# Optimization experiments

Measured on AMD Instinct MI355X. Metric: run time of the kernel, lower is better.

Reference implementation:

```python
import jax, jax.numpy as jnp
import numpy as np

U = 3      # kronecker_partitions
DP = 128   # kronecker_subdim
K = 32     # top_k_slots
B = 64


def setup_inputs() -> dict:
    key = jax.random.key(0)
    z = jax.random.normal(key, (B, U * DP), dtype=jnp.float32)
    log_tau = jnp.zeros((1,), dtype=jnp.float32)  # learned temperature param
    return {"z": z, "log_tau": log_tau}


def reference(z, log_tau):
    b = z.shape[0]
    parts = z.reshape(b, U, DP)                      # [B, U, d_p]
    tau = jnp.exp(log_tau)
    probs = jax.nn.softmax(parts / tau, axis=-1)     # per-partition softmax
    # Kronecker (outer) product across partitions -> [B, d_p^U]
    addr = probs[:, 0]
    for u in range(1, U):  # static loop over U=3 partitions
        addr = (addr[:, :, None] * probs[:, u][:, None, :]).reshape(b, -1)
    weights, indices = jax.lax.top_k(addr, K)        # [B, K] each
    return indices, weights
```

## Files before the change

### kernel.cpp

```cpp
#include <hip/hip_runtime.h>
#include <math.h>

namespace {

constexpr int NU    = 3;
constexpr int DPN   = 128;
constexpr int TOPK  = 32;
constexpr int NB    = 64;
constexpr int NCAND = 119;

__global__ __launch_bounds__(DPN) void kron_topk_kernel(
    const float* __restrict__ z, const float* __restrict__ log_tau,
    float* __restrict__ out) {
  const int row = blockIdx.x;
  const int tid = threadIdx.x;

  __shared__ __align__(16) float p[NU][DPN];
  __shared__ __align__(16) float red[NU][DPN];
  __shared__ float sval[NU][TOPK];
  __shared__ int   sidx[NU][TOPK];
  __shared__ __align__(16) float cval[DPN];
  __shared__ __align__(16) int   cidx[DPN];
  __shared__ float aval[TOPK];
  __shared__ int   aidx[TOPK];

  const float* zr = z + row * (NU * DPN);
  float x[NU];
#pragma unroll
  for (int u = 0; u < NU; ++u) x[u] = zr[u * DPN + tid];
  const float tau = expf(log_tau[0]);

  int rmap = 0, smap = 0;
  const bool cact = tid < NCAND;
  if (cact) {
    int t = tid, r = 0;
    while (true) {
      int cnt = TOPK / (r + 1);
      if (t < cnt) break;
      t -= cnt;
      ++r;
    }
    rmap = r;
    smap = t;
  }

  if (tau != 1.0f) {
#pragma unroll
    for (int u = 0; u < NU; ++u) x[u] /= tau;
  }
#pragma unroll
  for (int u = 0; u < NU; ++u) red[u][tid] = x[u];
  __syncthreads();
  for (int s = DPN / 2; s > 0; s >>= 1) {
    if (tid < s) {
#pragma unroll
      for (int u = 0; u < NU; ++u)
        red[u][tid] = fmaxf(red[u][tid], red[u][tid + s]);
    }
    __syncthreads();
  }
  float e[NU];
#pragma unroll
  for (int u = 0; u < NU; ++u) e[u] = expf(x[u] - red[u][0]);
  __syncthreads();
#pragma unroll
  for (int u = 0; u < NU; ++u) red[u][tid] = e[u];
  __syncthreads();
  for (int s = DPN / 2; s > 0; s >>= 1) {
    if (tid < s) {
#pragma unroll
      for (int u = 0; u < NU; ++u) red[u][tid] += red[u][tid + s];
    }
    __syncthreads();
  }
  float pv[NU];
#pragma unroll
  for (int u = 0; u < NU; ++u) {
    pv[u] = e[u] / red[u][0];
    p[u][tid] = pv[u];
  }
  __syncthreads();

  {
    int rk[NU] = {0, 0, 0};
    const float4* p4_0 = reinterpret_cast<const float4*>(&p[0][0]);
    const float4* p4_1 = reinterpret_cast<const float4*>(&p[1][0]);
    const float4* p4_2 = reinterpret_cast<const float4*>(&p[2][0]);
#pragma unroll 8
    for (int jj = 0; jj < DPN / 4; ++jj) {
      float4 w0 = p4_0[jj];
      float4 w1 = p4_1[jj];
      float4 w2 = p4_2[jj];
      const float* w0e = &w0.x;
      const float* w1e = &w1.x;
      const float* w2e = &w2.x;
#pragma unroll
      for (int ee = 0; ee < 4; ++ee) {
        int j = 4 * jj + ee;
        rk[0] += (w0e[ee] > pv[0]) || (w0e[ee] == pv[0] && j < tid);
        rk[1] += (w1e[ee] > pv[1]) || (w1e[ee] == pv[1] && j < tid);
        rk[2] += (w2e[ee] > pv[2]) || (w2e[ee] == pv[2] && j < tid);
      }
    }
#pragma unroll
    for (int u = 0; u < NU; ++u)
      if (rk[u] < TOPK) { sval[u][rk[u]] = pv[u]; sidx[u][rk[u]] = tid; }
  }
  __syncthreads();

  if (tid < TOPK) { aval[tid] = sval[0][tid]; aidx[tid] = sidx[0][tid]; }
  __syncthreads();

  for (int u = 1; u < NU; ++u) {
    float v = -1.0f;
    int idx = 0x7fffffff;
    if (cact) {
      v   = aval[rmap] * sval[u][smap];
      idx = aidx[rmap] * DPN + sidx[u][smap];
    }
    cval[tid] = v;
    cidx[tid] = idx;
    __syncthreads();

    int rank = 0;
    const float4* cv4 = reinterpret_cast<const float4*>(cval);
    const int4*   ci4 = reinterpret_cast<const int4*>(cidx);
#pragma unroll 8
    for (int jj = 0; jj < DPN / 4; ++jj) {
      float4 w4 = cv4[jj];
      int4   i4 = ci4[jj];
      const float* we = &w4.x;
      const int*   ie = &i4.x;
#pragma unroll
      for (int ee = 0; ee < 4; ++ee)
        rank += (we[ee] > v) || (we[ee] == v && ie[ee] < idx);
    }
    __syncthreads();
    if (rank < TOPK) { aval[rank] = v; aidx[rank] = idx; }
    __syncthreads();
  }

  if (tid < TOPK) {
    out[row * TOPK + tid]              = (float)aidx[tid];
    out[NB * TOPK + row * TOPK + tid]  = aval[tid];
  }
}

}

extern "C" void kernel_launch(void* const* d_in, const int* in_sizes, int n_in,
                              void* d_out, int out_size, void* d_ws, size_t ws_size,
                              hipStream_t stream) {
  const float* z       = (const float*)d_in[0];
  const float* log_tau = (const float*)d_in[1];
  float* out           = (float*)d_out;
  hipLaunchKernelGGL(kron_topk_kernel, dim3(NB), dim3(DPN), 0, stream,
                     z, log_tau, out);
}
```

Baseline: 75.29 us.

## Use wave shuffles for softmax reductions and single-wave candidate merge

Replaces the shared-memory tree reductions for per-partition max and sum with wavefront shuffle reductions, which removes many block barriers. After the per-partition top-k, the second wave exits and the first wave handles all 119 candidates alone, two per lane. Block-wide syncs are replaced with LDS waitcnt fences. This cuts barrier and latency overhead in a tiny latency-bound kernel, at the cost of doubling the per-lane rank work in the merge phase and relying on wave-synchronous LDS semantics.

```diff
diff --git a/kernel.cpp b/kernel.cpp
--- a/kernel.cpp
+++ b/kernel.cpp
@@ -9,14 +9,34 @@
 constexpr int NB    = 64;
 constexpr int NCAND = 119;
 
+__device__ __forceinline__ void lds_fence() {
+  asm volatile("s_waitcnt lgkmcnt(0)" ::: "memory");
+  __builtin_amdgcn_sched_barrier(0);
+}
+
+__device__ __forceinline__ void decode_rs(int c, int& r, int& s) {
+  int t = c, rr = 0;
+  while (true) {
+    int cnt = TOPK / (rr + 1);
+    if (t < cnt) break;
+    t -= cnt;
+    ++rr;
+  }
+  r = rr;
+  s = t;
+}
+
 __global__ __launch_bounds__(DPN) void kron_topk_kernel(
     const float* __restrict__ z, const float* __restrict__ log_tau,
     float* __restrict__ out) {
-  const int row = blockIdx.x;
-  const int tid = threadIdx.x;
+  const int row  = blockIdx.x;
+  const int tid  = threadIdx.x;
+  const int lane = tid & 63;
+  const int wid  = tid >> 6;
 
+  __shared__ __align__(16) float es[NU][DPN];
   __shared__ __align__(16) float p[NU][DPN];
-  __shared__ __align__(16) float red[NU][DPN];
+  __shared__ float mxs[NU][2];
   __shared__ float sval[NU][TOPK];
   __shared__ int   sidx[NU][TOPK];
   __shared__ __align__(16) float cval[DPN];
@@ -29,54 +49,40 @@
 #pragma unroll
   for (int u = 0; u < NU; ++u) x[u] = zr[u * DPN + tid];
   const float tau = expf(log_tau[0]);
-
-  int rmap = 0, smap = 0;
-  const bool cact = tid < NCAND;
-  if (cact) {
-    int t = tid, r = 0;
-    while (true) {
-      int cnt = TOPK / (r + 1);
-      if (t < cnt) break;
-      t -= cnt;
-      ++r;
-    }
-    rmap = r;
-    smap = t;
-  }
-
   if (tau != 1.0f) {
 #pragma unroll
     for (int u = 0; u < NU; ++u) x[u] /= tau;
   }
+
+  float mm[NU] = {x[0], x[1], x[2]};
 #pragma unroll
-  for (int u = 0; u < NU; ++u) red[u][tid] = x[u];
+  for (int d = 32; d > 0; d >>= 1) {
+#pragma unroll
+    for (int u = 0; u < NU; ++u) mm[u] = fmaxf(mm[u], __shfl_xor(mm[u], d));
+  }
+  if (lane == 0) {
+#pragma unroll
+    for (int u = 0; u < NU; ++u) mxs[u][wid] = mm[u];
+  }
   __syncthreads();
-  for (int s = DPN / 2; s > 0; s >>= 1) {
-    if (tid < s) {
-#pragma unroll
-      for (int u = 0; u < NU; ++u)
-        red[u][tid] = fmaxf(red[u][tid], red[u][tid + s]);
-    }
-    __syncthreads();
-  }
+
   float e[NU];
 #pragma unroll
-  for (int u = 0; u < NU; ++u) e[u] = expf(x[u] - red[u][0]);
+  for (int u = 0; u < NU; ++u) {
+    float m = fmaxf(mxs[u][0], mxs[u][1]);
+    e[u] = expf(x[u] - m);
+    es[u][tid] = e[u];
+  }
   __syncthreads();
-#pragma unroll
-  for (int u = 0; u < NU; ++u) red[u][tid] = e[u];
-  __syncthreads();
-  for (int s = DPN / 2; s > 0; s >>= 1) {
-    if (tid < s) {
-#pragma unroll
-      for (int u = 0; u < NU; ++u) red[u][tid] += red[u][tid + s];
-    }
-    __syncthreads();
-  }
+
   float pv[NU];
 #pragma unroll
   for (int u = 0; u < NU; ++u) {
-    pv[u] = e[u] / red[u][0];
+    float v = es[u][lane] + es[u][lane + 64];
+#pragma unroll
+    for (int d = 32; d > 0; d >>= 1) v += __shfl_xor(v, d);
+    float denom = __shfl(v, 0);
+    pv[u] = e[u] / denom;
     p[u][tid] = pv[u];
   }
   __syncthreads();
@@ -108,21 +114,33 @@
   }
   __syncthreads();
 
-  if (tid < TOPK) { aval[tid] = sval[0][tid]; aidx[tid] = sidx[0][tid]; }
-  __syncthreads();
+  if (wid == 1) return;
 
+  if (lane < TOPK) { aval[lane] = sval[0][lane]; aidx[lane] = sidx[0][lane]; }
+  lds_fence();
+
+  int r0, s0, r1 = 0, s1 = 0;
+  decode_rs(lane, r0, s0);
+  const bool has1 = (lane + 64) < NCAND;
+  if (has1) decode_rs(lane + 64, r1, s1);
+
+#pragma unroll
   for (int u = 1; u < NU; ++u) {
-    float v = -1.0f;
-    int idx = 0x7fffffff;
-    if (cact) {
-      v   = aval[rmap] * sval[u][smap];
-      idx = aidx[rmap] * DPN + sidx[u][smap];
+    float v0 = aval[r0] * sval[u][s0];
+    int   i0 = aidx[r0] * DPN + sidx[u][s0];
+    float v1 = -1.0f;
+    int   i1 = 0x7fffffff;
+    if (has1) {
+      v1 = aval[r1] * sval[u][s1];
+      i1 = aidx[r1] * DPN + sidx[u][s1];
     }
-    cval[tid] = v;
-    cidx[tid] = idx;
-    __syncthreads();
+    cval[lane]      = v0;
+    cidx[lane]      = i0;
+    cval[lane + 64] = v1;
+    cidx[lane + 64] = i1;
+    lds_fence();
 
-    int rank = 0;
+    int rk0 = 0, rk1 = 0;
     const float4* cv4 = reinterpret_cast<const float4*>(cval);
     const int4*   ci4 = reinterpret_cast<const int4*>(cidx);
 #pragma unroll 8
@@ -132,17 +150,20 @@
       const float* we = &w4.x;
       const int*   ie = &i4.x;
 #pragma unroll
-      for (int ee = 0; ee < 4; ++ee)
-        rank += (we[ee] > v) || (we[ee] == v && ie[ee] < idx);
+      for (int ee = 0; ee < 4; ++ee) {
+        rk0 += (we[ee] > v0) || (we[ee] == v0 && ie[ee] < i0);
+        rk1 += (we[ee] > v1) || (we[ee] == v1 && ie[ee] < i1);
+      }
     }
-    __syncthreads();
-    if (rank < TOPK) { aval[rank] = v; aidx[rank] = idx; }
-    __syncthreads();
+    lds_fence();
+    if (rk0 < TOPK)         { aval[rk0] = v0; aidx[rk0] = i0; }
+    if (has1 && rk1 < TOPK) { aval[rk1] = v1; aidx[rk1] = i1; }
+    lds_fence();
   }
 
-  if (tid < TOPK) {
-    out[row * TOPK + tid]              = (float)aidx[tid];
-    out[NB * TOPK + row * TOPK + tid]  = aval[tid];
+  if (lane < TOPK) {
+    out[row * TOPK + lane]             = (float)aidx[lane];
+    out[NB * TOPK + row * TOPK + lane] = aval[lane];
   }
 }
 
```

Result: no change. 75.59 us (+0.4%).
